# Performance work log

Hardware: AMD Instinct MI355X
Metric: run time of the kernel (lower is better)

The kernel has to match this reference:

```python
import jax, jax.numpy as jnp
import numpy as np

NUM_WIRES = 4
NUM_LAYERS = 2
BATCH = 1_048_576


def _rz(theta):
    # diag(e^{-i t/2}, e^{+i t/2})
    e = jnp.exp(-0.5j * theta.astype(jnp.complex64))
    z = jnp.zeros((), jnp.complex64)
    return jnp.stack([jnp.stack([e, z]), jnp.stack([z, jnp.conj(e)])])


def _rx(theta):
    c = jnp.cos(0.5 * theta).astype(jnp.complex64)
    s = (-1j * jnp.sin(0.5 * theta)).astype(jnp.complex64)
    return jnp.stack([jnp.stack([c, s]), jnp.stack([s, c])])


def _apply_1q(state, U, w):
    # state: (B,2,2,2,2); apply 2x2 unitary U on wire w (axis w+1)
    s = jnp.moveaxis(state, w + 1, -1)
    s = jnp.einsum('...i,ji->...j', s, U)
    return jnp.moveaxis(s, -1, w + 1)


def _cnot(state, c, t):
    # flip target axis where control bit == 1
    s = jnp.moveaxis(state, (c + 1, t + 1), (-2, -1))
    s = jnp.stack([s[..., 0, :], s[..., 1, ::-1]], axis=-2)
    return jnp.moveaxis(s, (-2, -1), (c + 1, t + 1))


def _circuit(x, params):
    # RY(x_i)|0> per wire gives product state [cos(x_i/2), sin(x_i/2)]
    h = 0.5 * x
    a = jnp.stack([jnp.cos(h), jnp.sin(h)], axis=-1).astype(jnp.complex64)  # (B,4,2)
    state = jnp.einsum('bi,bj,bk,bl->bijkl', a[:, 0], a[:, 1], a[:, 2], a[:, 3])
    for layer in range(NUM_LAYERS):
        for w in range(NUM_WIRES):
            # RZ then RX on wire w, fused into one 2x2 unitary
            U = _rx(params[layer, w, 1]) @ _rz(params[layer, w, 0])
            state = _apply_1q(state, U, w)
        for w in range(NUM_WIRES - 1):
            state = _cnot(state, w, w + 1)
        state = _cnot(state, NUM_WIRES - 1, 0)
    probs = state.real ** 2 + state.imag ** 2  # (B,2,2,2,2)
    evs = []
    for w in range(NUM_WIRES):
        axes = tuple(ax for ax in range(1, NUM_WIRES + 1) if ax != w + 1)
        p = jnp.sum(probs, axis=axes)  # (B,2) marginal of wire w
        evs.append(p[:, 0] - p[:, 1])  # <Z_w>
    return jnp.stack(evs, axis=-1)  # (B,4)


def setup_inputs() -> dict:
    key = jax.random.key(0)
    k1, k2 = jax.random.split(key)
    x = jax.random.normal(k1, (BATCH, NUM_WIRES), dtype=jnp.float32)
    params = jax.random.normal(k2, (NUM_LAYERS, NUM_WIRES, 2), dtype=jnp.float32)
    return {"x": x, "params": params}


def reference(x, params):
    return _circuit(x, params)
```

## Files before the change

kernel.cpp:

```cpp
#include <hip/hip_runtime.h>

#define NUM_WIRES 4
#define NUM_LAYERS 2


typedef __attribute__((address_space(4))) const float cfloat;

__global__ void gate_prep(const float* __restrict__ params, float* __restrict__ g) {
    const int t = threadIdx.x;
    if (t < 4) {
        const float p0 = params[t * 2 + 0];
        const float p1 = params[t * 2 + 1];
        float cz, sz, cx, sx;
        __sincosf(0.5f * p0, &sz, &cz);
        __sincosf(0.5f * p1, &sx, &cx);
        g[t * 4 + 0] = cx * cz;
        g[t * 4 + 1] = cx * sz;
        g[t * 4 + 2] = sx * sz;
        g[t * 4 + 3] = sx * cz;
    } else if (t < 8) {
        const int w = t - 4;
        const float p1 = params[(NUM_WIRES + w) * 2 + 1];
        float cx, sx;
        __sincosf(0.5f * p1, &sx, &cx);
        g[16 + w * 2] = cx;
        g[17 + w * 2] = sx;
    } else if (t >= 16 && t < 32) {
        const int i = t - 16;
        float dr = 1.f, di = 0.f;
        for (int w = 0; w < NUM_WIRES; ++w) {
            const float p0 = params[(NUM_WIRES + w) * 2 + 0];
            float c, s;
            __sincosf(0.5f * p0, &s, &c);
            const float sg = ((i >> (3 - w)) & 1) ? s : -s;
            const float ndr = dr * c - di * sg;
            const float ndi = dr * sg + di * c;
            dr = ndr; di = ndi;
        }
        g[24 + i * 2] = dr;
        g[25 + i * 2] = di;
    }
}

__device__ __forceinline__ void cmul(float ar, float ai, float br, float bi,
                                     float& orr, float& oi) {
    orr = fmaf(ar, br, -(ai * bi));
    oi  = fmaf(ar, bi,   ai * br);
}

template <int CM, int TM>
__device__ __forceinline__ void cnot(float zr[16], float zi[16]) {
#pragma unroll
    for (int i = 0; i < 16; ++i) {
        if ((i & CM) && !(i & TM)) {
            const int j = i | TM;
            float t;
            t = zr[i]; zr[i] = zr[j]; zr[j] = t;
            t = zi[i]; zi[i] = zi[j]; zi[j] = t;
        }
    }
}

__device__ __forceinline__ float4 sim_one(const float4 xv, cfloat* __restrict__ G) {
    float fr[4][2], fi[4][2];
    const float xs[4] = {xv.x, xv.y, xv.z, xv.w};
#pragma unroll
    for (int w = 0; w < 4; ++w) {
        float c, s;
        __sincosf(0.5f * xs[w], &s, &c);
        const float A = G[w * 4 + 0], B = G[w * 4 + 1];
        const float C = G[w * 4 + 2], D = G[w * 4 + 3];
        fr[w][0] = fmaf(A, c, C * s);
        fi[w][0] = fmaf(-B, c, -(D * s));
        fr[w][1] = fmaf(A, s, -(C * c));
        fi[w][1] = fmaf(B, s, -(D * c));
    }

    float mr[4], mi[4], nr[4], ni[4];
#pragma unroll
    for (int p = 0; p < 2; ++p)
#pragma unroll
        for (int q = 0; q < 2; ++q) {
            cmul(fr[0][p], fi[0][p], fr[1][q], fi[1][q], mr[p * 2 + q], mi[p * 2 + q]);
            cmul(fr[2][p], fi[2][p], fr[3][q], fi[3][q], nr[p * 2 + q], ni[p * 2 + q]);
        }
    float zr[16], zi[16];
#pragma unroll
    for (int i = 0; i < 16; ++i)
        cmul(mr[i >> 2], mi[i >> 2], nr[i & 3], ni[i & 3], zr[i], zi[i]);

    cnot<8, 4>(zr, zi);
    cnot<4, 2>(zr, zi);
    cnot<2, 1>(zr, zi);
    cnot<1, 8>(zr, zi);

#pragma unroll
    for (int i = 0; i < 16; ++i) {
        const float dr = G[24 + i * 2], di = G[25 + i * 2];
        const float ar = zr[i], ai = zi[i];
        zr[i] = fmaf(dr, ar, -(di * ai));
        zi[i] = fmaf(dr, ai,   di * ar);
    }

#pragma unroll
    for (int w = 0; w < 4; ++w) {
        const float c = G[16 + w * 2], s = G[17 + w * 2];
        const int M = 8 >> w;
#pragma unroll
        for (int i = 0; i < 16; ++i) {
            if (!(i & M)) {
                const int j = i | M;
                const float ar = zr[i], ai = zi[i];
                const float br = zr[j], bi = zi[j];
                zr[i] = fmaf(c, ar,   s * bi);
                zi[i] = fmaf(c, ai, -(s * br));
                zr[j] = fmaf(c, br,   s * ai);
                zi[j] = fmaf(c, bi, -(s * ar));
            }
        }
    }

    cnot<8, 4>(zr, zi);
    cnot<4, 2>(zr, zi);
    cnot<2, 1>(zr, zi);
    cnot<1, 8>(zr, zi);

    float p[16];
#pragma unroll
    for (int i = 0; i < 16; ++i) p[i] = fmaf(zr[i], zr[i], zi[i] * zi[i]);

    float d0[8], s1[8];
#pragma unroll
    for (int k = 0; k < 8; ++k) {
        d0[k] = p[2 * k] - p[2 * k + 1];
        s1[k] = p[2 * k] + p[2 * k + 1];
    }
    const float e3 = ((d0[0] + d0[1]) + (d0[2] + d0[3])) + ((d0[4] + d0[5]) + (d0[6] + d0[7]));
    const float e2 = ((s1[0] - s1[1]) + (s1[2] - s1[3])) + ((s1[4] - s1[5]) + (s1[6] - s1[7]));
    float s2[4];
#pragma unroll
    for (int k = 0; k < 4; ++k) s2[k] = s1[2 * k] + s1[2 * k + 1];
    const float e1 = (s2[0] - s2[1]) + (s2[2] - s2[3]);
    const float e0 = (s2[0] + s2[1]) - (s2[2] + s2[3]);

    return make_float4(e0, e1, e2, e3);
}

__global__ __launch_bounds__(256) void qsim_kernel(const float* __restrict__ x,
                                                   const float* __restrict__ gf,
                                                   float* __restrict__ out, int batch) {
    cfloat* G = (cfloat*)gf;

    const int tid = threadIdx.x;
    const int i0 = blockIdx.x * 512 + tid;
    const int i1 = i0 + 256;

    const float4 xa = (i0 < batch) ? reinterpret_cast<const float4*>(x)[i0]
                                   : make_float4(0.f, 0.f, 0.f, 0.f);
    const float4 xb = (i1 < batch) ? reinterpret_cast<const float4*>(x)[i1]
                                   : make_float4(0.f, 0.f, 0.f, 0.f);

    const float4 ra = sim_one(xa, G);
    const float4 rb = sim_one(xb, G);

    if (i0 < batch) reinterpret_cast<float4*>(out)[i0] = ra;
    if (i1 < batch) reinterpret_cast<float4*>(out)[i1] = rb;
}

extern "C" void kernel_launch(void* const* d_in, const int* in_sizes, int n_in,
                              void* d_out, int out_size, void* d_ws, size_t ws_size,
                              hipStream_t stream) {
    const float* x = (const float*)d_in[0];
    const float* params = (const float*)d_in[1];
    float* out = (float*)d_out;
    float* g = (float*)d_ws;
    const int batch = in_sizes[0] / NUM_WIRES;

    gate_prep<<<1, 64, 0, stream>>>(params, g);
    const int blocks = (batch + 511) / 512;
    qsim_kernel<<<blocks, 256, 0, stream>>>(x, g, out, batch);
}
```

Measured before the change: 83.76 us.

## Simulate two samples per thread in packed fp16 with hardware sin/cos

Moves the 16-amplitude statevector arithmetic from fp32 to packed half2. Each thread processes its two batch elements in the two lanes of every h2 register, so one packed fma does the work of two fp32 fmas. Gate coefficients are stored as replicated fp16 pairs, loaded once as vectors and made wave-uniform with readfirstlane. The angle evaluation switches to raw v_sin/v_cos with the angle pre-scaled by 1/(4π). The intent is to halve ALU instruction count, at the cost of fp16 precision in the state that may exceed the output tolerance.

```diff
diff --git a/kernel.cpp b/kernel.cpp
--- a/kernel.cpp
+++ b/kernel.cpp
@@ -4,9 +4,18 @@
 #define NUM_LAYERS 2
 
 
-typedef __attribute__((address_space(4))) const float cfloat;
-
-__global__ void gate_prep(const float* __restrict__ params, float* __restrict__ g) {
+#define INV_4PI 0.07957747154594767f
+
+typedef _Float16 h2 __attribute__((ext_vector_type(2)));
+
+__device__ __forceinline__ unsigned int rep16(float v) {
+    const _Float16 h = (_Float16)v;
+    unsigned short hs;
+    __builtin_memcpy(&hs, &h, 2);
+    return ((unsigned int)hs << 16) | hs;
+}
+
+__global__ void gate_prep(const float* __restrict__ params, unsigned int* __restrict__ g) {
     const int t = threadIdx.x;
     if (t < 4) {
         const float p0 = params[t * 2 + 0];
@@ -14,17 +23,17 @@
         float cz, sz, cx, sx;
         __sincosf(0.5f * p0, &sz, &cz);
         __sincosf(0.5f * p1, &sx, &cx);
-        g[t * 4 + 0] = cx * cz;
-        g[t * 4 + 1] = cx * sz;
-        g[t * 4 + 2] = sx * sz;
-        g[t * 4 + 3] = sx * cz;
+        g[t * 4 + 0] = rep16(cx * cz);
+        g[t * 4 + 1] = rep16(cx * sz);
+        g[t * 4 + 2] = rep16(sx * sz);
+        g[t * 4 + 3] = rep16(sx * cz);
     } else if (t < 8) {
         const int w = t - 4;
         const float p1 = params[(NUM_WIRES + w) * 2 + 1];
         float cx, sx;
         __sincosf(0.5f * p1, &sx, &cx);
-        g[16 + w * 2] = cx;
-        g[17 + w * 2] = sx;
+        g[16 + w * 2] = rep16(cx);
+        g[17 + w * 2] = rep16(sx);
     } else if (t >= 16 && t < 32) {
         const int i = t - 16;
         float dr = 1.f, di = 0.f;
@@ -37,46 +46,82 @@
             const float ndi = dr * sg + di * c;
             dr = ndr; di = ndi;
         }
-        g[24 + i * 2] = dr;
-        g[25 + i * 2] = di;
-    }
-}
-
-__device__ __forceinline__ void cmul(float ar, float ai, float br, float bi,
-                                     float& orr, float& oi) {
-    orr = fmaf(ar, br, -(ai * bi));
-    oi  = fmaf(ar, bi,   ai * br);
+        g[24 + i * 2] = rep16(dr);
+        g[25 + i * 2] = rep16(di);
+    }
+}
+
+__device__ __forceinline__ h2 ef(h2 a, h2 b, h2 c) { return __builtin_elementwise_fma(a, b, c); }
+
+__device__ __forceinline__ h2 u2h(unsigned int u) {
+    h2 r;
+    __builtin_memcpy(&r, &u, 4);
+    return r;
+}
+
+__device__ __forceinline__ void cmul(h2 ar, h2 ai, h2 br, h2 bi, h2& orr, h2& oi) {
+    orr = ef(ar, br, -(ai * bi));
+    oi  = ef(ar, bi,   ai * br);
 }
 
 template <int CM, int TM>
-__device__ __forceinline__ void cnot(float zr[16], float zi[16]) {
+__device__ __forceinline__ void cnot(h2 zr[16], h2 zi[16]) {
 #pragma unroll
     for (int i = 0; i < 16; ++i) {
         if ((i & CM) && !(i & TM)) {
             const int j = i | TM;
-            float t;
+            h2 t;
             t = zr[i]; zr[i] = zr[j]; zr[j] = t;
             t = zi[i]; zi[i] = zi[j]; zi[j] = t;
         }
     }
 }
 
-__device__ __forceinline__ float4 sim_one(const float4 xv, cfloat* __restrict__ G) {
-    float fr[4][2], fi[4][2];
-    const float xs[4] = {xv.x, xv.y, xv.z, xv.w};
-#pragma unroll
-    for (int w = 0; w < 4; ++w) {
-        float c, s;
-        __sincosf(0.5f * xs[w], &s, &c);
-        const float A = G[w * 4 + 0], B = G[w * 4 + 1];
-        const float C = G[w * 4 + 2], D = G[w * 4 + 3];
-        fr[w][0] = fmaf(A, c, C * s);
-        fi[w][0] = fmaf(-B, c, -(D * s));
-        fr[w][1] = fmaf(A, s, -(C * c));
-        fi[w][1] = fmaf(B, s, -(D * c));
-    }
-
-    float mr[4], mi[4], nr[4], ni[4];
+__global__ __launch_bounds__(256) void qsim_kernel(const float* __restrict__ x,
+                                                   const unsigned int* __restrict__ gu,
+                                                   float* __restrict__ out, int batch) {
+    const int tid = threadIdx.x;
+    const int i0 = blockIdx.x * 512 + tid;
+    const int i1 = i0 + 256;
+
+    h2 G[56];
+#pragma unroll
+    for (int k = 0; k < 14; ++k) {
+        const uint4 v = reinterpret_cast<const uint4*>(gu)[k];
+        G[4 * k + 0] = u2h((unsigned int)__builtin_amdgcn_readfirstlane((int)v.x));
+        G[4 * k + 1] = u2h((unsigned int)__builtin_amdgcn_readfirstlane((int)v.y));
+        G[4 * k + 2] = u2h((unsigned int)__builtin_amdgcn_readfirstlane((int)v.z));
+        G[4 * k + 3] = u2h((unsigned int)__builtin_amdgcn_readfirstlane((int)v.w));
+    }
+
+    const float4 xa = (i0 < batch) ? reinterpret_cast<const float4*>(x)[i0]
+                                   : make_float4(0.f, 0.f, 0.f, 0.f);
+    const float4 xb = (i1 < batch) ? reinterpret_cast<const float4*>(x)[i1]
+                                   : make_float4(0.f, 0.f, 0.f, 0.f);
+
+    h2 fr[4][2], fi[4][2];
+    {
+        const float axs[4] = {xa.x, xa.y, xa.z, xa.w};
+        const float bxs[4] = {xb.x, xb.y, xb.z, xb.w};
+#pragma unroll
+        for (int w = 0; w < 4; ++w) {
+            const float rA = axs[w] * INV_4PI;
+            const float rB = bxs[w] * INV_4PI;
+            h2 s, c;
+            s.x = (_Float16)__builtin_amdgcn_sinf(rA);
+            s.y = (_Float16)__builtin_amdgcn_sinf(rB);
+            c.x = (_Float16)__builtin_amdgcn_cosf(rA);
+            c.y = (_Float16)__builtin_amdgcn_cosf(rB);
+            const h2 A = G[w * 4 + 0], B = G[w * 4 + 1];
+            const h2 C = G[w * 4 + 2], D = G[w * 4 + 3];
+            fr[w][0] = ef(A, c, C * s);
+            fi[w][0] = ef(-B, c, -(D * s));
+            fr[w][1] = ef(A, s, -(C * c));
+            fi[w][1] = ef(B, s, -(D * c));
+        }
+    }
+
+    h2 mr[4], mi[4], nr[4], ni[4];
 #pragma unroll
     for (int p = 0; p < 2; ++p)
 #pragma unroll
@@ -84,7 +129,7 @@
             cmul(fr[0][p], fi[0][p], fr[1][q], fi[1][q], mr[p * 2 + q], mi[p * 2 + q]);
             cmul(fr[2][p], fi[2][p], fr[3][q], fi[3][q], nr[p * 2 + q], ni[p * 2 + q]);
         }
-    float zr[16], zi[16];
+    h2 zr[16], zi[16];
 #pragma unroll
     for (int i = 0; i < 16; ++i)
         cmul(mr[i >> 2], mi[i >> 2], nr[i & 3], ni[i & 3], zr[i], zi[i]);
@@ -96,26 +141,26 @@
 
 #pragma unroll
     for (int i = 0; i < 16; ++i) {
-        const float dr = G[24 + i * 2], di = G[25 + i * 2];
-        const float ar = zr[i], ai = zi[i];
-        zr[i] = fmaf(dr, ar, -(di * ai));
-        zi[i] = fmaf(dr, ai,   di * ar);
+        const h2 dr = G[24 + i * 2], di = G[25 + i * 2];
+        const h2 ar = zr[i], ai = zi[i];
+        zr[i] = ef(dr, ar, -(di * ai));
+        zi[i] = ef(dr, ai,   di * ar);
     }
 
 #pragma unroll
     for (int w = 0; w < 4; ++w) {
-        const float c = G[16 + w * 2], s = G[17 + w * 2];
+        const h2 c = G[16 + w * 2], s = G[17 + w * 2];
         const int M = 8 >> w;
 #pragma unroll
         for (int i = 0; i < 16; ++i) {
             if (!(i & M)) {
                 const int j = i | M;
-                const float ar = zr[i], ai = zi[i];
-                const float br = zr[j], bi = zi[j];
-                zr[i] = fmaf(c, ar,   s * bi);
-                zi[i] = fmaf(c, ai, -(s * br));
-                zr[j] = fmaf(c, br,   s * ai);
-                zi[j] = fmaf(c, bi, -(s * ar));
+                const h2 ar = zr[i], ai = zi[i];
+                const h2 br = zr[j], bi = zi[j];
+                zr[i] = ef(c, ar,   s * bi);
+                zi[i] = ef(c, ai, -(s * br));
+                zr[j] = ef(c, br,   s * ai);
+                zi[j] = ef(c, bi, -(s * ar));
             }
         }
     }
@@ -125,46 +170,34 @@
     cnot<2, 1>(zr, zi);
     cnot<1, 8>(zr, zi);
 
-    float p[16];
-#pragma unroll
-    for (int i = 0; i < 16; ++i) p[i] = fmaf(zr[i], zr[i], zi[i] * zi[i]);
-
-    float d0[8], s1[8];
-#pragma unroll
-    for (int k = 0; k < 8; ++k) {
-        d0[k] = p[2 * k] - p[2 * k + 1];
-        s1[k] = p[2 * k] + p[2 * k + 1];
-    }
-    const float e3 = ((d0[0] + d0[1]) + (d0[2] + d0[3])) + ((d0[4] + d0[5]) + (d0[6] + d0[7]));
-    const float e2 = ((s1[0] - s1[1]) + (s1[2] - s1[3])) + ((s1[4] - s1[5]) + (s1[6] - s1[7]));
-    float s2[4];
-#pragma unroll
-    for (int k = 0; k < 4; ++k) s2[k] = s1[2 * k] + s1[2 * k + 1];
-    const float e1 = (s2[0] - s2[1]) + (s2[2] - s2[3]);
-    const float e0 = (s2[0] + s2[1]) - (s2[2] + s2[3]);
-
-    return make_float4(e0, e1, e2, e3);
-}
-
-__global__ __launch_bounds__(256) void qsim_kernel(const float* __restrict__ x,
-                                                   const float* __restrict__ gf,
-                                                   float* __restrict__ out, int batch) {
-    cfloat* G = (cfloat*)gf;
-
-    const int tid = threadIdx.x;
-    const int i0 = blockIdx.x * 512 + tid;
-    const int i1 = i0 + 256;
-
-    const float4 xa = (i0 < batch) ? reinterpret_cast<const float4*>(x)[i0]
-                                   : make_float4(0.f, 0.f, 0.f, 0.f);
-    const float4 xb = (i1 < batch) ? reinterpret_cast<const float4*>(x)[i1]
-                                   : make_float4(0.f, 0.f, 0.f, 0.f);
-
-    const float4 ra = sim_one(xa, G);
-    const float4 rb = sim_one(xb, G);
-
-    if (i0 < batch) reinterpret_cast<float4*>(out)[i0] = ra;
-    if (i1 < batch) reinterpret_cast<float4*>(out)[i1] = rb;
+    float pA[16], pB[16];
+#pragma unroll
+    for (int i = 0; i < 16; ++i) {
+        const h2 p = ef(zr[i], zr[i], zi[i] * zi[i]);
+        pA[i] = (float)p.x;
+        pB[i] = (float)p.y;
+    }
+
+#pragma unroll
+    for (int e = 0; e < 2; ++e) {
+        const float* p = (e == 0) ? pA : pB;
+        float d0[8], s1[8];
+#pragma unroll
+        for (int k = 0; k < 8; ++k) {
+            d0[k] = p[2 * k] - p[2 * k + 1];
+            s1[k] = p[2 * k] + p[2 * k + 1];
+        }
+        const float e3 = ((d0[0] + d0[1]) + (d0[2] + d0[3])) + ((d0[4] + d0[5]) + (d0[6] + d0[7]));
+        const float e2 = ((s1[0] - s1[1]) + (s1[2] - s1[3])) + ((s1[4] - s1[5]) + (s1[6] - s1[7]));
+        float s2[4];
+#pragma unroll
+        for (int k = 0; k < 4; ++k) s2[k] = s1[2 * k] + s1[2 * k + 1];
+        const float e1 = (s2[0] - s2[1]) + (s2[2] - s2[3]);
+        const float e0 = (s2[0] + s2[1]) - (s2[2] + s2[3]);
+        const int idx = (e == 0) ? i0 : i1;
+        if (idx < batch)
+            reinterpret_cast<float4*>(out)[idx] = make_float4(e0, e1, e2, e3);
+    }
 }
 
 extern "C" void kernel_launch(void* const* d_in, const int* in_sizes, int n_in,
@@ -173,7 +206,7 @@
     const float* x = (const float*)d_in[0];
     const float* params = (const float*)d_in[1];
     float* out = (float*)d_out;
-    float* g = (float*)d_ws;
+    unsigned int* g = (unsigned int*)d_ws;
     const int batch = in_sizes[0] / NUM_WIRES;
 
     gate_prep<<<1, 64, 0, stream>>>(params, g);
```

New measurement: 79.11 us. 5.6% less time.
